# Performance work log

Measured on AMD Instinct MI355X. Metric: run time of the kernel, lower is better.

## Reference

```python
import jax, jax.numpy as jnp
import numpy as np
import math

N_HEADS = 16
D_MODEL = 1024
HEAD_DIM = D_MODEL // N_HEADS
ROPE_THETA = 10000.0


def _rope_cos_sin(seq_len, head_dim, dtype):
    # freqs = 1/theta^(2i/d), angles = outer(t, freqs)  -> [seq_len, head_dim//2]
    inv_freq = 1.0 / (ROPE_THETA ** (jnp.arange(0, head_dim, 2, dtype=jnp.float32) / head_dim))
    ang = jnp.arange(seq_len, dtype=jnp.float32)[:, None] * inv_freq[None, :]
    return jnp.cos(ang).astype(dtype), jnp.sin(ang).astype(dtype)


def _apply_rope(t, cos, sin):
    # t: [B, N, H, D]; treat last dim as complex pairs (a, b); multiply by e^{i*ang}
    B, N, H, D = t.shape
    tr = t.reshape(B, N, H, D // 2, 2)
    a, b = tr[..., 0], tr[..., 1]
    c = cos[None, :, None, :]  # [1, N, 1, D/2]
    s = sin[None, :, None, :]
    out = jnp.stack([a * c - b * s, a * s + b * c], axis=-1)
    return out.reshape(B, N, H, D)


def setup_inputs() -> dict:
    key = jax.random.key(0)
    ks = jax.random.split(key, 9)
    B, N, D = 4, 2048, D_MODEL
    scale = 0.02
    inp = {"x": jax.random.normal(ks[0], (B, N, D), dtype=jnp.float32)}
    for i, nm in enumerate(["q", "k", "v", "o"]):
        inp[f"w{nm}"] = jax.random.normal(ks[1 + 2 * i], (D, D), dtype=jnp.float32) * scale
        inp[f"b{nm}"] = jax.random.normal(ks[2 + 2 * i], (D,), dtype=jnp.float32) * scale
    return inp


def reference(x, wq, bq, wk, bk, wv, bv, wo, bo):
    B, N, D = x.shape
    H, Hd = N_HEADS, HEAD_DIM
    q = (x @ wq.T + bq).reshape(B, N, H, Hd)
    k = (x @ wk.T + bk).reshape(B, N, H, Hd)
    v = (x @ wv.T + bv).reshape(B, N, H, Hd)
    cos, sin = _rope_cos_sin(N, Hd, x.dtype)
    q = _apply_rope(q, cos, sin)
    k = _apply_rope(k, cos, sin)
    # SDPA, no mask, eval mode (dropout_p = 0)
    scores = jnp.einsum("bqhd,bkhd->bhqk", q, k) / math.sqrt(Hd)
    attn = jax.nn.softmax(scores, axis=-1)
    out = jnp.einsum("bhqk,bkhd->bqhd", attn, v)  # [B, N, H, Hd]
    out = out.reshape(B, N, D)
    return out @ wo.T + bo
```

## Files before the change

kernel.cpp:

```cpp
#include <hip/hip_runtime.h>
#include <math.h>
#include <stdint.h>

#define BBATCH 4
#define NTOK   2048
#define DMOD   1024
#define NH     16
#define HD     64
#define MTOT   8192

typedef __bf16 bf16;
typedef __bf16 bf16x2 __attribute__((ext_vector_type(2)));
typedef __bf16 bf16x4 __attribute__((ext_vector_type(4)));
typedef __bf16 bf16x8 __attribute__((ext_vector_type(8)));
typedef float  f32x4  __attribute__((ext_vector_type(4)));
typedef float  f32x16 __attribute__((ext_vector_type(16)));
typedef unsigned int u32;
typedef unsigned int u32x2 __attribute__((ext_vector_type(2)));
typedef unsigned int u32x4 __attribute__((ext_vector_type(4)));

typedef __attribute__((address_space(3))) unsigned int lds_u32;
typedef __attribute__((address_space(1))) unsigned int glb_u32;

__device__ __forceinline__ void gload16(const bf16* g, bf16* l) {
    __builtin_amdgcn_global_load_lds((glb_u32*)g, (lds_u32*)l, 16, 0, 0);
}

__device__ __forceinline__ u32 pack_bf16(float lo, float hi) {
    bf16x2 z; z[0] = (bf16)lo; z[1] = (bf16)hi;
    return __builtin_bit_cast(u32, z);
}

__device__ __forceinline__ float vsum16(f32x16 v) {
    float a0 = v[0] + v[1],   a1 = v[2] + v[3];
    float a2 = v[4] + v[5],   a3 = v[6] + v[7];
    float a4 = v[8] + v[9],   a5 = v[10] + v[11];
    float a6 = v[12] + v[13], a7 = v[14] + v[15];
    float b0 = a0 + a1, b1 = a2 + a3, b2 = a4 + a5, b3 = a6 + a7;
    return (b0 + b1) + (b2 + b3);
}

#define MFMA32(a, b, c) __builtin_amdgcn_mfma_f32_32x32x16_bf16((a), (b), (c), 0, 0, 0)

#define QSCALE 0.1803368801111204f

__global__ __launch_bounds__(256)
void convert_kernel(const float* __restrict__ x,  const float* __restrict__ wq,
                    const float* __restrict__ wk, const float* __restrict__ wv,
                    const float* __restrict__ wo,
                    bf16* __restrict__ xb,  bf16* __restrict__ wqb,
                    bf16* __restrict__ wkb, bf16* __restrict__ wvb,
                    bf16* __restrict__ wob,
                    float* __restrict__ ct, float* __restrict__ st)
{
    if (blockIdx.x < 256) {
        int idx = blockIdx.x * 256 + threadIdx.x;
        int n = idx >> 5, p = idx & 31;
        float inv = powf(10000.0f, -(float)(2 * p) / 64.0f);
        float ang = (float)n * inv;
        ct[idx] = cosf(ang);
        st[idx] = sinf(ang);
    }

    const int X4 = (MTOT * DMOD) / 4;
    const int W4 = (DMOD * DMOD) / 4;
    int i = blockIdx.x * 256 + threadIdx.x;
    const float* src; bf16* dst; int off;
    if (i < X4) { src = x; dst = xb; off = i; }
    else {
        int j = i - X4; int w = j / W4; off = j - w * W4;
        src = (w == 0) ? wq : (w == 1) ? wk : (w == 2) ? wv : wo;
        dst = (w == 0) ? wqb : (w == 1) ? wkb : (w == 2) ? wvb : wob;
    }
    float4 v = ((const float4*)src)[off];
    bf16x4 o;
    o[0] = (bf16)v.x; o[1] = (bf16)v.y; o[2] = (bf16)v.z; o[3] = (bf16)v.w;
    *(bf16x4*)(dst + (size_t)off * 4) = o;
}

__global__ __launch_bounds__(512)
void gemm_qkv(const bf16* __restrict__ A,
              const bf16* __restrict__ wq, const bf16* __restrict__ wk,
              const bf16* __restrict__ wv,
              const float* __restrict__ bq, const float* __restrict__ bk,
              const float* __restrict__ bv,
              bf16* __restrict__ qb, bf16* __restrict__ kb, bf16* __restrict__ vtb,
              const float* __restrict__ ct, const float* __restrict__ st)
{
    __shared__ __align__(16) bf16 As[2][256 * 32];
    __shared__ __align__(16) bf16 Bs[2][128 * 32];

    const int sel = blockIdx.x >> 3;
    const int n0  = (blockIdx.x & 7) * 128;
    const int m0  = blockIdx.y * 256;
    const bf16*  W    = (sel == 0) ? wq : (sel == 1) ? wk : wv;
    const float* bias = (sel == 0) ? bq : (sel == 1) ? bk : bv;
    bf16*        out  = (sel == 0) ? qb : (sel == 1) ? kb : vtb;

    const int tid = threadIdx.x;
    const int l   = tid & 63;
    const int wid = tid >> 6;
    const int wm  = wid >> 1, wn = wid & 1;
    const int fr  = l & 15, fg = l >> 4;

    const int srow  = tid >> 2;
    const int sslot = (tid & 3) ^ ((srow >> 1) & 3);
    const bf16* gA0 = A + (size_t)(m0 + srow) * 1024 + sslot * 8;
    const bf16* gB0 = W + (size_t)(n0 + srow) * 1024 + sslot * 8;

    const int aswz = (fg ^ ((fr >> 1) & 3)) * 8;
    int aoff[4], boff[4];
#pragma unroll
    for (int i = 0; i < 4; ++i) {
        aoff[i] = (wm * 64 + i * 16 + fr) * 32 + aswz;
        boff[i] = (wn * 64 + i * 16 + fr) * 32 + aswz;
    }

    f32x4 acc[4][4] = {};

#define QSTAGE(kt, b) do {                                           \
        const bf16* a0_ = gA0 + (kt) * 32;                           \
        const bf16* b0_ = gB0 + (kt) * 32;                           \
        gload16(a0_,                       As[b] + tid * 8);         \
        gload16(a0_ + (size_t)128 * 1024,  As[b] + 4096 + tid * 8);  \
        gload16(b0_,                       Bs[b] + tid * 8);         \
    } while (0)

    QSTAGE(0, 0);
    __syncthreads();
    int cur = 0;

    for (int kt = 0; kt < 32; ++kt) {
        if (kt < 31) QSTAGE(kt + 1, cur ^ 1);

        bf16x8 af[4], bfv[4];
#pragma unroll
        for (int i = 0; i < 4; ++i) af[i]  = *(const bf16x8*)(As[cur] + aoff[i]);
#pragma unroll
        for (int i = 0; i < 4; ++i) bfv[i] = *(const bf16x8*)(Bs[cur] + boff[i]);
#pragma unroll
        for (int mi = 0; mi < 4; ++mi)
#pragma unroll
            for (int ni = 0; ni < 4; ++ni)
                acc[mi][ni] = __builtin_amdgcn_mfma_f32_16x16x32_bf16(
                    af[mi], bfv[ni], acc[mi][ni], 0, 0, 0);

        __syncthreads();
        cur ^= 1;
    }
#undef QSTAGE

    if (sel == 2) {
#pragma unroll
        for (int ni = 0; ni < 4; ++ni) {
            const int col = n0 + wn * 64 + ni * 16 + fr;
            const int h = col >> 6, dd = col & 63;
            const float bvv = bias[col];
#pragma unroll
            for (int mi = 0; mi < 4; ++mi) {
                const int rowb = m0 + wm * 64 + mi * 16 + fg * 4;
                const int bi = rowb >> 11, npb = rowb & (NTOK - 1);
                bf16x4 ov;
#pragma unroll
                for (int r = 0; r < 4; ++r) ov[r] = (bf16)(acc[mi][ni][r] + bvv);
                *(bf16x4*)(out + ((size_t)(bi * NH + h) * HD + dd) * NTOK + npb) = ov;
            }
        }
    } else {
        const float scale = (sel == 0) ? QSCALE : 1.0f;
#pragma unroll
        for (int ni = 0; ni < 4; ++ni) {
            const int col = n0 + wn * 64 + ni * 16 + fr;
            const int h = col >> 6, dd = col & 63, p = (dd >> 1);
            const float bvv = bias[col];
#pragma unroll
            for (int mi = 0; mi < 4; ++mi) {
                const int rowb = m0 + wm * 64 + mi * 16 + fg * 4;
#pragma unroll
                for (int r = 0; r < 4; ++r) {
                    const int row = rowb + r;
                    const int bi = row >> 11, np = row & (NTOK - 1);
                    float v  = acc[mi][ni][r] + bvv;
                    float pv = __shfl_xor(v, 1);
                    float c = ct[np * 32 + p], s = st[np * 32 + p];
                    float o = (dd & 1) ? (pv * s + v * c) : (v * c - pv * s);
                    o *= scale;
                    out[((size_t)(bi * NH + h) * NTOK + np) * HD + dd] = (bf16)o;
                }
            }
        }
    }
}

__global__ __launch_bounds__(256)
void gemm_oproj(const bf16* __restrict__ A, const bf16* __restrict__ W,
                const float* __restrict__ bias, float* __restrict__ out)
{
    __shared__ __align__(16) bf16 As[2][128 * 32];
    __shared__ __align__(16) bf16 Bs[2][128 * 32];

    const int m0 = blockIdx.y * 128, n0 = blockIdx.x * 128;
    const int tid = threadIdx.x;
    const int l   = tid & 63;
    const int wid = tid >> 6;
    const int wm  = wid >> 1, wn = wid & 1;
    const int fr  = l & 15, fg = l >> 4;

    const int srow  = tid >> 2;
    const int sslot = (tid & 3) ^ ((srow >> 1) & 3);
    const bf16* gA0 = A + (size_t)(m0 + srow) * 1024 + sslot * 8;
    const bf16* gB0 = W + (size_t)(n0 + srow) * 1024 + sslot * 8;

    const int aswz = (fg ^ ((fr >> 1) & 3)) * 8;
    int aoff[4], boff[4];
#pragma unroll
    for (int i = 0; i < 4; ++i) {
        aoff[i] = (wm * 64 + i * 16 + fr) * 32 + aswz;
        boff[i] = (wn * 64 + i * 16 + fr) * 32 + aswz;
    }

    f32x4 acc[4][4] = {};

#define OSTAGE(kt, b) do {                                          \
        const bf16* a0_ = gA0 + (kt) * 32;                          \
        const bf16* b0_ = gB0 + (kt) * 32;                          \
        gload16(a0_,                      As[b] + tid * 8);         \
        gload16(a0_ + (size_t)64 * 1024,  As[b] + 2048 + tid * 8);  \
        gload16(b0_,                      Bs[b] + tid * 8);         \
        gload16(b0_ + (size_t)64 * 1024,  Bs[b] + 2048 + tid * 8);  \
    } while (0)

    OSTAGE(0, 0);
    __syncthreads();
    int cur = 0;

    for (int kt = 0; kt < 32; ++kt) {
        if (kt < 31) OSTAGE(kt + 1, cur ^ 1);

        bf16x8 af[4], bfv[4];
#pragma unroll
        for (int i = 0; i < 4; ++i) af[i]  = *(const bf16x8*)(As[cur] + aoff[i]);
#pragma unroll
        for (int i = 0; i < 4; ++i) bfv[i] = *(const bf16x8*)(Bs[cur] + boff[i]);
#pragma unroll
        for (int mi = 0; mi < 4; ++mi)
#pragma unroll
            for (int ni = 0; ni < 4; ++ni)
                acc[mi][ni] = __builtin_amdgcn_mfma_f32_16x16x32_bf16(
                    af[mi], bfv[ni], acc[mi][ni], 0, 0, 0);

        __syncthreads();
        cur ^= 1;
    }
#undef OSTAGE

#pragma unroll
    for (int ni = 0; ni < 4; ++ni) {
        const int col = n0 + wn * 64 + ni * 16 + fr;
        const float bv = bias[col];
#pragma unroll
        for (int mi = 0; mi < 4; ++mi) {
            const int rowb = m0 + wm * 64 + mi * 16 + fg * 4;
#pragma unroll
            for (int r = 0; r < 4; ++r)
                out[(size_t)(rowb + r) * 1024 + col] = acc[mi][ni][r] + bv;
        }
    }
}

__global__ __launch_bounds__(256, 2)
void attn_mfma(const bf16* __restrict__ Q, const bf16* __restrict__ K,
               const bf16* __restrict__ Vt, bf16* __restrict__ out)
{
    __shared__ __align__(16) bf16 Ks[2][64 * 64];
    __shared__ __align__(16) bf16 Vs[2][64 * 64];

    const int tid = threadIdx.x;
    const int l   = tid & 63;
    const int wid = tid >> 6;
    const int lq  = l & 31;
    const int hi  = l >> 5;
    const int rx  = lq & 7;
    const int q0 = blockIdx.x * 256;
    const int bh = blockIdx.y;

    const bf16* Qb = Q  + (size_t)bh * NTOK * HD;
    const bf16* Kb = K  + (size_t)bh * NTOK * HD;
    const bf16* Vb = Vt + (size_t)bh * HD * NTOK;

    const int qbase = q0 + wid * 64;
    bf16x8 qf0[4], qf1[4];
#pragma unroll
    for (int c = 0; c < 4; ++c) {
        qf0[c] = *(const bf16x8*)(Qb + (size_t)(qbase + lq) * HD + c * 16 + hi * 8);
        qf1[c] = *(const bf16x8*)(Qb + (size_t)(qbase + 32 + lq) * HD + c * 16 + hi * 8);
    }

    const int srow  = tid >> 3;
    const int sslot = (tid & 7) ^ (srow & 7);
    const bf16* gK0 = Kb + (size_t)srow * HD + sslot * 8;
    const bf16* gV0 = Vb + (size_t)srow * NTOK + sslot * 8;

#define ASTAGE(t, b) do {                                          \
        const bf16* gK_ = gK0 + (size_t)(t) * 64 * HD;             \
        const bf16* gV_ = gV0 + (size_t)(t) * 64;                  \
        gload16(gK_,                      Ks[b] + tid * 8);        \
        gload16(gK_ + 32 * HD,            Ks[b] + 2048 + tid * 8); \
        gload16(gV_,                      Vs[b] + tid * 8);        \
        gload16(gV_ + (size_t)32 * NTOK,  Vs[b] + 2048 + tid * 8); \
    } while (0)

    f32x16 oA0 = {}, oA1 = {};
    f32x16 oB0 = {}, oB1 = {};
    float lsA = 0.f, lsB = 0.f;

    ASTAGE(0, 0);
    __syncthreads();
    int cur = 0;

    for (int t = 0; t < 32; ++t) {
        if (t < 31) ASTAGE(t + 1, cur ^ 1);
        const bf16* Kc = Ks[cur];
        const bf16* Vc = Vs[cur];

        bf16x8 kf0[4], kf1[4];
#pragma unroll
        for (int c = 0; c < 4; ++c) {
            const int slot = ((c * 2 + hi) ^ rx) * 8;
            kf0[c] = *(const bf16x8*)(Kc + lq * 64 + slot);
            kf1[c] = *(const bf16x8*)(Kc + (32 + lq) * 64 + slot);
        }

        bf16x8 pfA[4], pfB[4];

        {
            f32x16 t0 = {}, t1 = {};
#pragma unroll
            for (int c = 0; c < 4; ++c) {
                t0 = MFMA32(kf0[c], qf0[c], t0);
                t1 = MFMA32(kf1[c], qf0[c], t1);
            }
#pragma unroll
            for (int r = 0; r < 16; ++r) t0[r] = __builtin_amdgcn_exp2f(t0[r]);
#pragma unroll
            for (int r = 0; r < 16; ++r) t1[r] = __builtin_amdgcn_exp2f(t1[r]);
            lsA += vsum16(t0) + vsum16(t1);
#pragma unroll
            for (int b = 0; b < 2; ++b) {
                const f32x16& tb = b ? t1 : t0;
#pragma unroll
                for (int kc = 0; kc < 2; ++kc) {
                    const int a0 = kc ? 8 : 0, a1 = kc ? 12 : 4;
                    u32 X  = pack_bf16(tb[a0],     tb[a0 + 1]);
                    u32 Y  = pack_bf16(tb[a1],     tb[a1 + 1]);
                    u32 X2 = pack_bf16(tb[a0 + 2], tb[a0 + 3]);
                    u32 Y2 = pack_bf16(tb[a1 + 2], tb[a1 + 3]);
                    u32x2 s0 = __builtin_amdgcn_permlane32_swap(X,  Y,  false, false);
                    u32x2 s1 = __builtin_amdgcn_permlane32_swap(X2, Y2, false, false);
                    u32x4 bw;
                    bw[0] = s0[0]; bw[1] = s1[0]; bw[2] = s0[1]; bw[3] = s1[1];
                    pfA[b * 2 + kc] = __builtin_bit_cast(bf16x8, bw);
                }
            }
        }

        {
            f32x16 t0 = {}, t1 = {};
#pragma unroll
            for (int c = 0; c < 4; ++c) {
                t0 = MFMA32(kf0[c], qf1[c], t0);
                t1 = MFMA32(kf1[c], qf1[c], t1);
            }
#pragma unroll
            for (int r = 0; r < 16; ++r) t0[r] = __builtin_amdgcn_exp2f(t0[r]);
#pragma unroll
            for (int r = 0; r < 16; ++r) t1[r] = __builtin_amdgcn_exp2f(t1[r]);
            lsB += vsum16(t0) + vsum16(t1);
#pragma unroll
            for (int b = 0; b < 2; ++b) {
                const f32x16& tb = b ? t1 : t0;
#pragma unroll
                for (int kc = 0; kc < 2; ++kc) {
                    const int a0 = kc ? 8 : 0, a1 = kc ? 12 : 4;
                    u32 X  = pack_bf16(tb[a0],     tb[a0 + 1]);
                    u32 Y  = pack_bf16(tb[a1],     tb[a1 + 1]);
                    u32 X2 = pack_bf16(tb[a0 + 2], tb[a0 + 3]);
                    u32 Y2 = pack_bf16(tb[a1 + 2], tb[a1 + 3]);
                    u32x2 s0 = __builtin_amdgcn_permlane32_swap(X,  Y,  false, false);
                    u32x2 s1 = __builtin_amdgcn_permlane32_swap(X2, Y2, false, false);
                    u32x4 bw;
                    bw[0] = s0[0]; bw[1] = s1[0]; bw[2] = s0[1]; bw[3] = s1[1];
                    pfB[b * 2 + kc] = __builtin_bit_cast(bf16x8, bw);
                }
            }
        }

        bf16x8 vf0[4], vf1[4];
#pragma unroll
        for (int j = 0; j < 4; ++j) {
            const int slot = ((j * 2 + hi) ^ rx) * 8;
            vf0[j] = *(const bf16x8*)(Vc + lq * 64 + slot);
            vf1[j] = *(const bf16x8*)(Vc + (32 + lq) * 64 + slot);
        }
#pragma unroll
        for (int j = 0; j < 4; ++j) {
            oA0 = MFMA32(vf0[j], pfA[j], oA0);
            oA1 = MFMA32(vf1[j], pfA[j], oA1);
            oB0 = MFMA32(vf0[j], pfB[j], oB0);
            oB1 = MFMA32(vf1[j], pfB[j], oB1);
        }

        __syncthreads();
        cur ^= 1;
    }
#undef ASTAGE

    const int b_ = bh >> 4, h = bh & 15;
    const float lA = lsA + __shfl_xor(lsA, 32);
    const float lB = lsB + __shfl_xor(lsB, 32);
    const float invA = 1.0f / lA;
    const float invB = 1.0f / lB;

    {
        const int token = qbase + lq;
        bf16* dst = out + (size_t)(b_ * NTOK + token) * DMOD + h * HD;
#pragma unroll
        for (int dblk = 0; dblk < 2; ++dblk) {
            const f32x16& ob = dblk ? oA1 : oA0;
#pragma unroll
            for (int g = 0; g < 4; ++g) {
                bf16x4 ov;
#pragma unroll
                for (int r2 = 0; r2 < 4; ++r2) ov[r2] = (bf16)(ob[g * 4 + r2] * invA);
                *(bf16x4*)(dst + dblk * 32 + g * 8 + hi * 4) = ov;
            }
        }
    }
    {
        const int token = qbase + 32 + lq;
        bf16* dst = out + (size_t)(b_ * NTOK + token) * DMOD + h * HD;
#pragma unroll
        for (int dblk = 0; dblk < 2; ++dblk) {
            const f32x16& ob = dblk ? oB1 : oB0;
#pragma unroll
            for (int g = 0; g < 4; ++g) {
                bf16x4 ov;
#pragma unroll
                for (int r2 = 0; r2 < 4; ++r2) ov[r2] = (bf16)(ob[g * 4 + r2] * invB);
                *(bf16x4*)(dst + dblk * 32 + g * 8 + hi * 4) = ov;
            }
        }
    }
}

extern "C" void kernel_launch(void* const* d_in, const int* in_sizes, int n_in,
                              void* d_out, int out_size, void* d_ws, size_t ws_size,
                              hipStream_t stream)
{
    (void)in_sizes; (void)n_in; (void)out_size; (void)ws_size;

    const float* x  = (const float*)d_in[0];
    const float* wq = (const float*)d_in[1];
    const float* bq = (const float*)d_in[2];
    const float* wk = (const float*)d_in[3];
    const float* bk = (const float*)d_in[4];
    const float* wv = (const float*)d_in[5];
    const float* bv = (const float*)d_in[6];
    const float* wo = (const float*)d_in[7];
    const float* bo = (const float*)d_in[8];
    float* out = (float*)d_out;

    const size_t XSZ = (size_t)MTOT * DMOD;
    const size_t WSZ = (size_t)DMOD * DMOD;
    bf16* xb  = (bf16*)d_ws;
    bf16* wqb = xb  + XSZ;
    bf16* wkb = wqb + WSZ;
    bf16* wvb = wkb + WSZ;
    bf16* wob = wvb + WSZ;
    bf16* qb  = wob + WSZ;
    bf16* kb  = qb  + XSZ;
    bf16* vtb = kb  + XSZ;
    bf16* ab  = vtb + XSZ;
    float* ct = (float*)(ab + XSZ);
    float* st = ct + (size_t)NTOK * 32;

    convert_kernel<<<dim3(12288), dim3(256), 0, stream>>>(x, wq, wk, wv, wo,
                                                          xb, wqb, wkb, wvb, wob,
                                                          ct, st);

    gemm_qkv<<<dim3(24, MTOT / 256), dim3(512), 0, stream>>>(
        xb, wqb, wkb, wvb, bq, bk, bv, qb, kb, vtb, ct, st);

    attn_mfma<<<dim3(NTOK / 256, BBATCH * NH), dim3(256), 0, stream>>>(qb, kb, vtb, ab);

    gemm_oproj<<<dim3(DMOD / 128, MTOT / 128), dim3(256), 0, stream>>>(ab, wob, bo, out);
}
```

Baseline: 297.4 us.

## Triple-buffer QKV and output-projection GEMM tiles with explicit vmcnt waits

Both projection GEMMs move from double-buffered to triple-buffered LDS staging, prefetching two K-tiles ahead. Fine-grained s_waitcnt vmcnt counts replace the full __syncthreads so a wave waits only for the tile it is about to consume, which keeps more global loads in flight across iterations. This costs 50% more shared memory per block, which may lower occupancy, and the hand-coded vmcnt values depend on exactly how many loads each stage issues.

```diff
diff --git a/kernel.cpp b/kernel.cpp
--- a/kernel.cpp
+++ b/kernel.cpp
@@ -87,8 +87,8 @@
               bf16* __restrict__ qb, bf16* __restrict__ kb, bf16* __restrict__ vtb,
               const float* __restrict__ ct, const float* __restrict__ st)
 {
-    __shared__ __align__(16) bf16 As[2][256 * 32];
-    __shared__ __align__(16) bf16 Bs[2][128 * 32];
+    __shared__ __align__(16) bf16 As[3][256 * 32];
+    __shared__ __align__(16) bf16 Bs[3][128 * 32];
 
     const int sel = blockIdx.x >> 3;
     const int n0  = (blockIdx.x & 7) * 128;
@@ -127,11 +127,19 @@
     } while (0)
 
     QSTAGE(0, 0);
-    __syncthreads();
+    QSTAGE(1, 1);
     int cur = 0;
 
     for (int kt = 0; kt < 32; ++kt) {
-        if (kt < 31) QSTAGE(kt + 1, cur ^ 1);
+        int nxt = cur + 2; if (nxt >= 3) nxt -= 3;
+        if (kt < 30) QSTAGE(kt + 2, nxt);
+
+        if (kt < 30)      asm volatile("s_waitcnt vmcnt(6)");
+        else if (kt == 30) asm volatile("s_waitcnt vmcnt(3)");
+        else               asm volatile("s_waitcnt vmcnt(0)");
+        __builtin_amdgcn_sched_barrier(0);
+        __builtin_amdgcn_s_barrier();
+        __builtin_amdgcn_sched_barrier(0);
 
         bf16x8 af[4], bfv[4];
 #pragma unroll
@@ -145,8 +153,10 @@
                 acc[mi][ni] = __builtin_amdgcn_mfma_f32_16x16x32_bf16(
                     af[mi], bfv[ni], acc[mi][ni], 0, 0, 0);
 
-        __syncthreads();
-        cur ^= 1;
+        asm volatile("s_waitcnt lgkmcnt(0)");
+        __builtin_amdgcn_sched_barrier(0);
+        __builtin_amdgcn_s_barrier();
+        cur = (cur == 2) ? 0 : cur + 1;
     }
 #undef QSTAGE
 
@@ -196,8 +206,8 @@
 void gemm_oproj(const bf16* __restrict__ A, const bf16* __restrict__ W,
                 const float* __restrict__ bias, float* __restrict__ out)
 {
-    __shared__ __align__(16) bf16 As[2][128 * 32];
-    __shared__ __align__(16) bf16 Bs[2][128 * 32];
+    __shared__ __align__(16) bf16 As[3][128 * 32];
+    __shared__ __align__(16) bf16 Bs[3][128 * 32];
 
     const int m0 = blockIdx.y * 128, n0 = blockIdx.x * 128;
     const int tid = threadIdx.x;
@@ -231,11 +241,19 @@
     } while (0)
 
     OSTAGE(0, 0);
-    __syncthreads();
+    OSTAGE(1, 1);
     int cur = 0;
 
     for (int kt = 0; kt < 32; ++kt) {
-        if (kt < 31) OSTAGE(kt + 1, cur ^ 1);
+        int nxt = cur + 2; if (nxt >= 3) nxt -= 3;
+        if (kt < 30) OSTAGE(kt + 2, nxt);
+
+        if (kt < 30)      asm volatile("s_waitcnt vmcnt(8)");
+        else if (kt == 30) asm volatile("s_waitcnt vmcnt(4)");
+        else               asm volatile("s_waitcnt vmcnt(0)");
+        __builtin_amdgcn_sched_barrier(0);
+        __builtin_amdgcn_s_barrier();
+        __builtin_amdgcn_sched_barrier(0);
 
         bf16x8 af[4], bfv[4];
 #pragma unroll
@@ -249,8 +267,10 @@
                 acc[mi][ni] = __builtin_amdgcn_mfma_f32_16x16x32_bf16(
                     af[mi], bfv[ni], acc[mi][ni], 0, 0, 0);
 
-        __syncthreads();
-        cur ^= 1;
+        asm volatile("s_waitcnt lgkmcnt(0)");
+        __builtin_amdgcn_sched_barrier(0);
+        __builtin_amdgcn_s_barrier();
+        cur = (cur == 2) ? 0 : cur + 1;
     }
 #undef OSTAGE
 
```

Result: slower. 310.0 us (+4.2%).
